# Performance work log

Measured on AMD Instinct MI355X. Metric: run time of the kernel, lower is better.

## Reference

```python
import jax, jax.numpy as jnp
import numpy as np


def _pairwise_l2(set1, set2):
    # set1: [B, N, C], set2: [B, M, C] -> [B, N, M] Euclidean distances.
    # Equivalent to ||a - b||_2 computed via the expanded quadratic form,
    # avoiding the O(B*N*M*C) broadcasted-difference intermediate.
    sq1 = jnp.sum(set1 * set1, axis=-1)  # [B, N]
    sq2 = jnp.sum(set2 * set2, axis=-1)  # [B, M]
    inner = jnp.einsum('bnc,bmc->bnm', set1, set2)  # [B, N, M]
    d2 = sq1[:, :, None] + sq2[:, None, :] - 2.0 * inner
    return jnp.sqrt(jnp.maximum(d2, 0.0))


def reference(set1, set2):
    # mode == Hausdorff.average
    if set1.ndim == 2:
        set1 = set1[None]
    if set2.ndim == 2:
        set2 = set2[None]
    distances = _pairwise_l2(set1, set2)  # [B, N, M]
    term_1 = jnp.mean(jnp.min(distances, axis=2), axis=1)  # [B]
    term_2 = jnp.mean(jnp.min(distances, axis=1), axis=1)  # [B]
    res = term_1 + term_2
    if res.shape[0] == 1:
        res = jnp.squeeze(res, axis=0)
    return res


def setup_inputs() -> dict:
    key = jax.random.key(0)
    k1, k2 = jax.random.split(key)
    B, N, M, C = 8, 4096, 4096, 128
    set1 = jax.random.normal(k1, (B, N, C), dtype=jnp.float32)
    set2 = jax.random.normal(k2, (B, M, C), dtype=jnp.float32)
    return {"set1": set1, "set2": set2}
```

## Files before the change

### kernel.cpp

```cpp
#include <hip/hip_runtime.h>

#define B_ 8
#define N_ 4096
#define M_ 4096
#define C_ 128
#define BN_ (B_ * N_)
#define BM_ (B_ * M_)

typedef __attribute__((ext_vector_type(8))) short bf16x8;
typedef __attribute__((ext_vector_type(4))) float floatx4;
typedef __attribute__((ext_vector_type(8))) unsigned short ushort8;

__device__ __forceinline__ unsigned short f2bf(float x) {
    unsigned int u = __float_as_uint(x);
    u += 0x7FFFu + ((u >> 16) & 1u);
    return (unsigned short)(u >> 16);
}

__device__ __forceinline__ void gl2lds16(const void* g, void* l) {
    __builtin_amdgcn_global_load_lds(
        (const __attribute__((address_space(1))) void*)g,
        (__attribute__((address_space(3))) void*)l, 16, 0, 0);
}

__global__ __launch_bounds__(256) void prep_kernel(
    const float* __restrict__ S1, const float* __restrict__ S2,
    unsigned int* __restrict__ minbuf, float* __restrict__ norms,
    unsigned short* __restrict__ bfA, unsigned short* __restrict__ bfB,
    float* __restrict__ out) {
    const int lane = threadIdx.x & 63;
    const int w    = threadIdx.x >> 6;
    const int gw   = blockIdx.x * 4 + w;
    const int r4   = lane >> 4;
    const int g4   = lane & 15;
    const int row  = gw * 4 + r4;

    const float* src = (row < BN_) ? S1 + (size_t)row * C_
                                   : S2 + (size_t)(row - BN_) * C_;
    float4 v0 = ((const float4*)src)[g4 * 2];
    float4 v1 = ((const float4*)src)[g4 * 2 + 1];

    float s = v0.x*v0.x + v0.y*v0.y + v0.z*v0.z + v0.w*v0.w
            + v1.x*v1.x + v1.y*v1.y + v1.z*v1.z + v1.w*v1.w;
    s += __shfl_xor(s, 1, 64);
    s += __shfl_xor(s, 2, 64);
    s += __shfl_xor(s, 4, 64);
    s += __shfl_xor(s, 8, 64);

    ushort8 o;
    o[0] = f2bf(v0.x); o[1] = f2bf(v0.y); o[2] = f2bf(v0.z); o[3] = f2bf(v0.w);
    o[4] = f2bf(v1.x); o[5] = f2bf(v1.y); o[6] = f2bf(v1.z); o[7] = f2bf(v1.w);

    unsigned short* dst = (row < BN_) ? bfA + (size_t)row * C_
                                      : bfB + (size_t)(row - BN_) * C_;
    *(ushort8*)&dst[(g4 ^ (row & 15)) * 8] = o;

    if (g4 == 0) { norms[row] = s; minbuf[row] = 0x7F800000u; }
    if (blockIdx.x == 0 && threadIdx.x < B_) out[threadIdx.x] = 0.f;
}

__global__ __launch_bounds__(256, 2) void hausdorff_mfma(
    const unsigned short* __restrict__ Abf, const unsigned short* __restrict__ Bbf,
    const float* __restrict__ asq_g, const float* __restrict__ bsq_g,
    unsigned int* __restrict__ rowmin, unsigned int* __restrict__ colmin) {

    __shared__ unsigned short B_lds[2][64 * 128];

    const int b     = blockIdx.z;
    const int row0  = blockIdx.x * 128;
    const int panel = blockIdx.y;
    const int tid   = threadIdx.x;
    const int lane  = tid & 63;
    const int w     = tid >> 6;
    const int lm    = lane & 15;
    const int quad  = lane >> 4;
    const int wrow  = (w >> 1) * 64;
    const int qc    = (w & 1) * 32;

    const unsigned short* Aws = Abf + ((size_t)b * N_ + row0) * C_;
    const unsigned short* Bws = Bbf + ((size_t)b * M_ + panel * 1024) * C_;

    #pragma unroll
    for (int k = 0; k < 4; ++k) {
        const int off = w * 2048 + k * 512;
        gl2lds16(Aws + off + lane * 8,        &B_lds[0][off]);
        gl2lds16(Aws + 8192 + off + lane * 8, &B_lds[1][off]);
    }

    float sa[16];
    #pragma unroll
    for (int i = 0; i < 4; ++i) {
        float4 t = *(const float4*)&asq_g[(size_t)b * N_ + row0 + wrow + 16 * i + 4 * quad];
        sa[4*i+0] = t.x; sa[4*i+1] = t.y; sa[4*i+2] = t.z; sa[4*i+3] = t.w;
    }

    float rv[16];
    #pragma unroll
    for (int v = 0; v < 16; ++v) rv[v] = 1e30f;

    __syncthreads();

    bf16x8 af[4][4];
    {
        const unsigned short* Abuf = &B_lds[w >> 1][0];
        #pragma unroll
        for (int i = 0; i < 4; ++i)
            #pragma unroll
            for (int c = 0; c < 4; ++c)
                af[i][c] = *(const bf16x8*)
                    &Abuf[(16 * i + lm) * 128 + (((c * 4 + quad) ^ lm) * 8)];
    }

    __syncthreads();

    #pragma unroll
    for (int k = 0; k < 4; ++k) {
        const int off = w * 2048 + k * 512;
        gl2lds16(Bws + off + lane * 8, &B_lds[0][off]);
    }
    __syncthreads();

    for (int it = 0; it < 16; ++it) {
        const int cur = it & 1;
        if (it < 15) {
            const unsigned short* Bt = Bws + (size_t)(it + 1) * 64 * C_;
            #pragma unroll
            for (int k = 0; k < 4; ++k) {
                const int off = w * 2048 + k * 512;
                gl2lds16(Bt + off + lane * 8, &B_lds[cur ^ 1][off]);
            }
        }
        const int colbase = panel * 1024 + it * 64;
        const float sb0 = bsq_g[(size_t)b * M_ + colbase + qc + lm];
        const float sb1 = bsq_g[(size_t)b * M_ + colbase + qc + 16 + lm];

        bf16x8 bf[2][4];
        #pragma unroll
        for (int j = 0; j < 2; ++j)
            #pragma unroll
            for (int c = 0; c < 4; ++c)
                bf[j][c] = *(const bf16x8*)
                    &B_lds[cur][(qc + 16 * j + lm) * 128 + (((c * 4 + quad) ^ lm) * 8)];

        floatx4 acc[4][2] = {};
        #pragma unroll
        for (int c = 0; c < 4; ++c)
            #pragma unroll
            for (int i = 0; i < 4; ++i)
                #pragma unroll
                for (int j = 0; j < 2; ++j)
                    acc[i][j] = __builtin_amdgcn_mfma_f32_16x16x32_bf16(
                        af[i][c], bf[j][c], acc[i][j], 0, 0, 0);

        float cv0 = 1e30f, cv1 = 1e30f;
        #pragma unroll
        for (int i = 0; i < 4; ++i)
            #pragma unroll
            for (int reg = 0; reg < 4; ++reg) {
                const int v = 4 * i + reg;
                float d0 = fmaf(-2.0f, acc[i][0][reg], sa[v] + sb0);
                float d1 = fmaf(-2.0f, acc[i][1][reg], sa[v] + sb1);
                rv[v] = fminf(rv[v], fminf(d0, d1));
                cv0 = fminf(cv0, d0);
                cv1 = fminf(cv1, d1);
            }
        cv0 = fminf(cv0, __shfl_xor(cv0, 16, 64));
        cv0 = fminf(cv0, __shfl_xor(cv0, 32, 64));
        cv1 = fminf(cv1, __shfl_xor(cv1, 16, 64));
        cv1 = fminf(cv1, __shfl_xor(cv1, 32, 64));
        if (quad == 0) {
            atomicMin(&colmin[(size_t)b * M_ + colbase + qc + lm],
                      __float_as_uint(fmaxf(cv0, 0.f)));
            atomicMin(&colmin[(size_t)b * M_ + colbase + qc + 16 + lm],
                      __float_as_uint(fmaxf(cv1, 0.f)));
        }
        __syncthreads();
    }

    #pragma unroll
    for (int s = 1; s < 16; s <<= 1)
        #pragma unroll
        for (int v = 0; v < 16; ++v)
            rv[v] = fminf(rv[v], __shfl_xor(rv[v], s, 64));
    if (lm == 0) {
        #pragma unroll
        for (int v = 0; v < 16; ++v)
            atomicMin(&rowmin[(size_t)b * N_ + row0 + wrow + 16 * (v >> 2) +
                              4 * quad + (v & 3)],
                      __float_as_uint(fmaxf(rv[v], 0.f)));
    }
}

__global__ __launch_bounds__(256) void hausdorff_reduce(
    const unsigned int* __restrict__ rowmin,
    const unsigned int* __restrict__ colmin, float* __restrict__ out) {
    __shared__ float ws4[4];
    const int b    = blockIdx.x >> 3;
    const int part = blockIdx.x & 7;
    const int base = part * 512;
    float s = 0.f;
    for (int i = base + threadIdx.x; i < base + 512; i += 256)
        s += sqrtf(fmaxf(__uint_as_float(rowmin[(size_t)b * N_ + i]), 0.f)) * (1.f / N_)
           + sqrtf(fmaxf(__uint_as_float(colmin[(size_t)b * M_ + i]), 0.f)) * (1.f / M_);
    #pragma unroll
    for (int off = 32; off > 0; off >>= 1) s += __shfl_down(s, off, 64);
    if ((threadIdx.x & 63) == 0) ws4[threadIdx.x >> 6] = s;
    __syncthreads();
    if (threadIdx.x == 0)
        atomicAdd(&out[b], ws4[0] + ws4[1] + ws4[2] + ws4[3]);
}

extern "C" void kernel_launch(void* const* d_in, const int* in_sizes, int n_in,
                              void* d_out, int out_size, void* d_ws, size_t ws_size,
                              hipStream_t stream) {
    const float* s1 = (const float*)d_in[0];
    const float* s2 = (const float*)d_in[1];
    float* out = (float*)d_out;

    unsigned int* rowmin = (unsigned int*)d_ws;
    unsigned int* colmin = rowmin + BN_;
    float* norms         = (float*)(colmin + BM_);
    unsigned short* bfA  = (unsigned short*)(norms + BN_ + BM_);
    unsigned short* bfB  = bfA + (size_t)BN_ * C_;

    prep_kernel<<<(BN_ + BM_) / 16, 256, 0, stream>>>(
        s1, s2, rowmin, norms, bfA, bfB, out);

    dim3 grid(N_ / 128, M_ / 1024, B_);
    hausdorff_mfma<<<grid, 256, 0, stream>>>(
        bfA, bfB, norms, norms + BN_, rowmin, colmin);

    hausdorff_reduce<<<B_ * 8, 256, 0, stream>>>(rowmin, colmin, out);
}
```

Measured before the change: 123.0 us.

## Fold norms into MFMA accumulator init, buffer column mins in LDS, fuse final reduce

The accumulators now start at -0.5*(|a|^2+|b|^2), so the MFMA directly produces a scaled negative squared distance. The epilogue becomes plain max operations instead of fma plus min. Per-tile column-min atomics go to an LDS buffer, which is flushed to global memory once per block, cutting global atomic traffic by 16x. A last-block-done counter per batch performs the final sqrt-mean reduction inside the main kernel, removing the third launch. The cost is a serialized tail reduction in one block per batch, plus the extra fence and counter logic.

```diff
diff --git a/kernel.cpp b/kernel.cpp
--- a/kernel.cpp
+++ b/kernel.cpp
@@ -27,7 +27,7 @@
     const float* __restrict__ S1, const float* __restrict__ S2,
     unsigned int* __restrict__ minbuf, float* __restrict__ norms,
     unsigned short* __restrict__ bfA, unsigned short* __restrict__ bfB,
-    float* __restrict__ out) {
+    float* __restrict__ out, unsigned int* __restrict__ done) {
     const int lane = threadIdx.x & 63;
     const int w    = threadIdx.x >> 6;
     const int gw   = blockIdx.x * 4 + w;
@@ -56,15 +56,22 @@
     *(ushort8*)&dst[(g4 ^ (row & 15)) * 8] = o;
 
     if (g4 == 0) { norms[row] = s; minbuf[row] = 0x7F800000u; }
-    if (blockIdx.x == 0 && threadIdx.x < B_) out[threadIdx.x] = 0.f;
+    if (blockIdx.x == 0 && threadIdx.x < B_) {
+        out[threadIdx.x] = 0.f;
+        done[threadIdx.x] = 0u;
+    }
 }
 
 __global__ __launch_bounds__(256, 2) void hausdorff_mfma(
     const unsigned short* __restrict__ Abf, const unsigned short* __restrict__ Bbf,
     const float* __restrict__ asq_g, const float* __restrict__ bsq_g,
-    unsigned int* __restrict__ rowmin, unsigned int* __restrict__ colmin) {
+    unsigned int* __restrict__ rowmin, unsigned int* __restrict__ colmin,
+    float* __restrict__ out, unsigned int* __restrict__ done_ctr) {
 
     __shared__ unsigned short B_lds[2][64 * 128];
+    __shared__ unsigned int colbuf[16 * 64];
+    __shared__ unsigned int s_last;
+    __shared__ float ws4[4];
 
     const int b     = blockIdx.z;
     const int row0  = blockIdx.x * 128;
@@ -87,16 +94,20 @@
         gl2lds16(Aws + 8192 + off + lane * 8, &B_lds[1][off]);
     }
 
-    float sa[16];
+    #pragma unroll
+    for (int e = 0; e < 4; ++e) colbuf[tid * 4 + e] = 0x7F800000u;
+
+    float sah[16];
     #pragma unroll
     for (int i = 0; i < 4; ++i) {
         float4 t = *(const float4*)&asq_g[(size_t)b * N_ + row0 + wrow + 16 * i + 4 * quad];
-        sa[4*i+0] = t.x; sa[4*i+1] = t.y; sa[4*i+2] = t.z; sa[4*i+3] = t.w;
+        sah[4*i+0] = -0.5f * t.x; sah[4*i+1] = -0.5f * t.y;
+        sah[4*i+2] = -0.5f * t.z; sah[4*i+3] = -0.5f * t.w;
     }
 
     float rv[16];
     #pragma unroll
-    for (int v = 0; v < 16; ++v) rv[v] = 1e30f;
+    for (int v = 0; v < 16; ++v) rv[v] = -1e30f;
 
     __syncthreads();
 
@@ -131,8 +142,8 @@
             }
         }
         const int colbase = panel * 1024 + it * 64;
-        const float sb0 = bsq_g[(size_t)b * M_ + colbase + qc + lm];
-        const float sb1 = bsq_g[(size_t)b * M_ + colbase + qc + 16 + lm];
+        const float nb0 = -0.5f * bsq_g[(size_t)b * M_ + colbase + qc + lm];
+        const float nb1 = -0.5f * bsq_g[(size_t)b * M_ + colbase + qc + 16 + lm];
 
         bf16x8 bf[2][4];
         #pragma unroll
@@ -142,7 +153,15 @@
                 bf[j][c] = *(const bf16x8*)
                     &B_lds[cur][(qc + 16 * j + lm) * 128 + (((c * 4 + quad) ^ lm) * 8)];
 
-        floatx4 acc[4][2] = {};
+        floatx4 acc[4][2];
+        #pragma unroll
+        for (int i = 0; i < 4; ++i)
+            #pragma unroll
+            for (int reg = 0; reg < 4; ++reg) {
+                acc[i][0][reg] = sah[4*i+reg] + nb0;
+                acc[i][1][reg] = sah[4*i+reg] + nb1;
+            }
+
         #pragma unroll
         for (int c = 0; c < 4; ++c)
             #pragma unroll
@@ -152,62 +171,75 @@
                     acc[i][j] = __builtin_amdgcn_mfma_f32_16x16x32_bf16(
                         af[i][c], bf[j][c], acc[i][j], 0, 0, 0);
 
-        float cv0 = 1e30f, cv1 = 1e30f;
-        #pragma unroll
-        for (int i = 0; i < 4; ++i)
-            #pragma unroll
-            for (int reg = 0; reg < 4; ++reg) {
-                const int v = 4 * i + reg;
-                float d0 = fmaf(-2.0f, acc[i][0][reg], sa[v] + sb0);
-                float d1 = fmaf(-2.0f, acc[i][1][reg], sa[v] + sb1);
-                rv[v] = fminf(rv[v], fminf(d0, d1));
-                cv0 = fminf(cv0, d0);
-                cv1 = fminf(cv1, d1);
-            }
-        cv0 = fminf(cv0, __shfl_xor(cv0, 16, 64));
-        cv0 = fminf(cv0, __shfl_xor(cv0, 32, 64));
-        cv1 = fminf(cv1, __shfl_xor(cv1, 16, 64));
-        cv1 = fminf(cv1, __shfl_xor(cv1, 32, 64));
+        float cv0 = -1e30f, cv1 = -1e30f;
+        #pragma unroll
+        for (int i = 0; i < 4; ++i) {
+            #pragma unroll
+            for (int reg = 0; reg < 4; ++reg)
+                rv[4*i+reg] = fmaxf(rv[4*i+reg],
+                                    fmaxf(acc[i][0][reg], acc[i][1][reg]));
+            cv0 = fmaxf(cv0, fmaxf(fmaxf(acc[i][0][0], acc[i][0][1]),
+                                   fmaxf(acc[i][0][2], acc[i][0][3])));
+            cv1 = fmaxf(cv1, fmaxf(fmaxf(acc[i][1][0], acc[i][1][1]),
+                                   fmaxf(acc[i][1][2], acc[i][1][3])));
+        }
+        cv0 = fmaxf(cv0, __shfl_xor(cv0, 16, 64));
+        cv0 = fmaxf(cv0, __shfl_xor(cv0, 32, 64));
+        cv1 = fmaxf(cv1, __shfl_xor(cv1, 16, 64));
+        cv1 = fmaxf(cv1, __shfl_xor(cv1, 32, 64));
         if (quad == 0) {
-            atomicMin(&colmin[(size_t)b * M_ + colbase + qc + lm],
-                      __float_as_uint(fmaxf(cv0, 0.f)));
-            atomicMin(&colmin[(size_t)b * M_ + colbase + qc + 16 + lm],
-                      __float_as_uint(fmaxf(cv1, 0.f)));
+            atomicMin(&colbuf[it * 64 + qc + lm],
+                      __float_as_uint(fmaxf(-2.0f * cv0, 0.f)));
+            atomicMin(&colbuf[it * 64 + qc + 16 + lm],
+                      __float_as_uint(fmaxf(-2.0f * cv1, 0.f)));
         }
         __syncthreads();
     }
 
     #pragma unroll
+    for (int e = 0; e < 4; ++e) {
+        const int idx = tid * 4 + e;
+        atomicMin(&colmin[(size_t)b * M_ + panel * 1024 + idx], colbuf[idx]);
+    }
+
+    #pragma unroll
     for (int s = 1; s < 16; s <<= 1)
         #pragma unroll
         for (int v = 0; v < 16; ++v)
-            rv[v] = fminf(rv[v], __shfl_xor(rv[v], s, 64));
+            rv[v] = fmaxf(rv[v], __shfl_xor(rv[v], s, 64));
     if (lm == 0) {
         #pragma unroll
         for (int v = 0; v < 16; ++v)
             atomicMin(&rowmin[(size_t)b * N_ + row0 + wrow + 16 * (v >> 2) +
                               4 * quad + (v & 3)],
-                      __float_as_uint(fmaxf(rv[v], 0.f)));
-    }
-}
-
-__global__ __launch_bounds__(256) void hausdorff_reduce(
-    const unsigned int* __restrict__ rowmin,
-    const unsigned int* __restrict__ colmin, float* __restrict__ out) {
-    __shared__ float ws4[4];
-    const int b    = blockIdx.x >> 3;
-    const int part = blockIdx.x & 7;
-    const int base = part * 512;
-    float s = 0.f;
-    for (int i = base + threadIdx.x; i < base + 512; i += 256)
-        s += sqrtf(fmaxf(__uint_as_float(rowmin[(size_t)b * N_ + i]), 0.f)) * (1.f / N_)
-           + sqrtf(fmaxf(__uint_as_float(colmin[(size_t)b * M_ + i]), 0.f)) * (1.f / M_);
-    #pragma unroll
-    for (int off = 32; off > 0; off >>= 1) s += __shfl_down(s, off, 64);
-    if ((threadIdx.x & 63) == 0) ws4[threadIdx.x >> 6] = s;
-    __syncthreads();
-    if (threadIdx.x == 0)
-        atomicAdd(&out[b], ws4[0] + ws4[1] + ws4[2] + ws4[3]);
+                      __float_as_uint(fmaxf(-2.0f * rv[v], 0.f)));
+    }
+
+    __syncthreads();
+    if (tid == 0) {
+        __threadfence();
+        s_last = (atomicAdd(&done_ctr[b], 1u) == 127u) ? 1u : 0u;
+    }
+    __syncthreads();
+    if (s_last) {
+        __threadfence();
+        float s = 0.f;
+        for (int i = tid; i < N_; i += 256) {
+            unsigned int ur = __hip_atomic_load(&rowmin[(size_t)b * N_ + i],
+                                                __ATOMIC_RELAXED,
+                                                __HIP_MEMORY_SCOPE_AGENT);
+            unsigned int uc = __hip_atomic_load(&colmin[(size_t)b * M_ + i],
+                                                __ATOMIC_RELAXED,
+                                                __HIP_MEMORY_SCOPE_AGENT);
+            s += sqrtf(fmaxf(__uint_as_float(ur), 0.f)) * (1.f / N_)
+               + sqrtf(fmaxf(__uint_as_float(uc), 0.f)) * (1.f / M_);
+        }
+        #pragma unroll
+        for (int off = 32; off > 0; off >>= 1) s += __shfl_down(s, off, 64);
+        if ((tid & 63) == 0) ws4[tid >> 6] = s;
+        __syncthreads();
+        if (tid == 0) out[b] = ws4[0] + ws4[1] + ws4[2] + ws4[3];
+    }
 }
 
 extern "C" void kernel_launch(void* const* d_in, const int* in_sizes, int n_in,
@@ -222,13 +254,12 @@
     float* norms         = (float*)(colmin + BM_);
     unsigned short* bfA  = (unsigned short*)(norms + BN_ + BM_);
     unsigned short* bfB  = bfA + (size_t)BN_ * C_;
+    unsigned int* done   = (unsigned int*)(bfB + (size_t)BM_ * C_);
 
     prep_kernel<<<(BN_ + BM_) / 16, 256, 0, stream>>>(
-        s1, s2, rowmin, norms, bfA, bfB, out);
+        s1, s2, rowmin, norms, bfA, bfB, out, done);
 
     dim3 grid(N_ / 128, M_ / 1024, B_);
     hausdorff_mfma<<<grid, 256, 0, stream>>>(
-        bfA, bfB, norms, norms + BN_, rowmin, colmin);
-
-    hausdorff_reduce<<<B_ * 8, 256, 0, stream>>>(rowmin, colmin, out);
-}
+        bfA, bfB, norms, norms + BN_, rowmin, colmin, out, done);
+}
```

Result: slower. 151.3 us (+23.0%).

## Buffer column minima in LDS and fuse final reduction via last-block counter

Applied to the files above, without the earlier changes.

Column minima from each tile are now stored in shared memory across all 16 iterations and merged once per block, so each block issues one atomicMin per column instead of two per 64-column tile per wave pair. The separate reduce kernel is removed: a per-batch completion counter lets the last finishing block compute the sqrt-mean sum and write the output. This removes a kernel launch and cuts global atomic traffic, in exchange for 8 KB more LDS per block (which may affect occupancy) and a serialized tail reduction done by one block per batch.

```diff
diff --git a/kernel.cpp b/kernel.cpp
--- a/kernel.cpp
+++ b/kernel.cpp
@@ -27,7 +27,7 @@
     const float* __restrict__ S1, const float* __restrict__ S2,
     unsigned int* __restrict__ minbuf, float* __restrict__ norms,
     unsigned short* __restrict__ bfA, unsigned short* __restrict__ bfB,
-    float* __restrict__ out) {
+    float* __restrict__ out, unsigned int* __restrict__ done) {
     const int lane = threadIdx.x & 63;
     const int w    = threadIdx.x >> 6;
     const int gw   = blockIdx.x * 4 + w;
@@ -56,15 +56,22 @@
     *(ushort8*)&dst[(g4 ^ (row & 15)) * 8] = o;
 
     if (g4 == 0) { norms[row] = s; minbuf[row] = 0x7F800000u; }
-    if (blockIdx.x == 0 && threadIdx.x < B_) out[threadIdx.x] = 0.f;
+    if (blockIdx.x == 0 && threadIdx.x < B_) {
+        out[threadIdx.x] = 0.f;
+        done[threadIdx.x] = 0u;
+    }
 }
 
 __global__ __launch_bounds__(256, 2) void hausdorff_mfma(
     const unsigned short* __restrict__ Abf, const unsigned short* __restrict__ Bbf,
     const float* __restrict__ asq_g, const float* __restrict__ bsq_g,
-    unsigned int* __restrict__ rowmin, unsigned int* __restrict__ colmin) {
+    unsigned int* __restrict__ rowmin, unsigned int* __restrict__ colmin,
+    float* __restrict__ out, unsigned int* __restrict__ done_ctr) {
 
     __shared__ unsigned short B_lds[2][64 * 128];
+    __shared__ unsigned int colbuf2[2][16 * 64];
+    unsigned int* s_last = &colbuf2[1][0];
+    float* ws4 = (float*)&colbuf2[0][0];
 
     const int b     = blockIdx.z;
     const int row0  = blockIdx.x * 128;
@@ -169,12 +176,17 @@
         cv1 = fminf(cv1, __shfl_xor(cv1, 16, 64));
         cv1 = fminf(cv1, __shfl_xor(cv1, 32, 64));
         if (quad == 0) {
-            atomicMin(&colmin[(size_t)b * M_ + colbase + qc + lm],
-                      __float_as_uint(fmaxf(cv0, 0.f)));
-            atomicMin(&colmin[(size_t)b * M_ + colbase + qc + 16 + lm],
-                      __float_as_uint(fmaxf(cv1, 0.f)));
+            colbuf2[w >> 1][it * 64 + qc + lm]      = __float_as_uint(fmaxf(cv0, 0.f));
+            colbuf2[w >> 1][it * 64 + qc + 16 + lm] = __float_as_uint(fmaxf(cv1, 0.f));
         }
         __syncthreads();
+    }
+
+    #pragma unroll
+    for (int e = 0; e < 4; ++e) {
+        const int idx = tid * 4 + e;
+        const unsigned int m = min(colbuf2[0][idx], colbuf2[1][idx]);
+        atomicMin(&colmin[(size_t)b * M_ + panel * 1024 + idx], m);
     }
 
     #pragma unroll
@@ -189,25 +201,33 @@
                               4 * quad + (v & 3)],
                       __float_as_uint(fmaxf(rv[v], 0.f)));
     }
-}
-
-__global__ __launch_bounds__(256) void hausdorff_reduce(
-    const unsigned int* __restrict__ rowmin,
-    const unsigned int* __restrict__ colmin, float* __restrict__ out) {
-    __shared__ float ws4[4];
-    const int b    = blockIdx.x >> 3;
-    const int part = blockIdx.x & 7;
-    const int base = part * 512;
-    float s = 0.f;
-    for (int i = base + threadIdx.x; i < base + 512; i += 256)
-        s += sqrtf(fmaxf(__uint_as_float(rowmin[(size_t)b * N_ + i]), 0.f)) * (1.f / N_)
-           + sqrtf(fmaxf(__uint_as_float(colmin[(size_t)b * M_ + i]), 0.f)) * (1.f / M_);
-    #pragma unroll
-    for (int off = 32; off > 0; off >>= 1) s += __shfl_down(s, off, 64);
-    if ((threadIdx.x & 63) == 0) ws4[threadIdx.x >> 6] = s;
-    __syncthreads();
-    if (threadIdx.x == 0)
-        atomicAdd(&out[b], ws4[0] + ws4[1] + ws4[2] + ws4[3]);
+
+    __syncthreads();
+    if (tid == 0) {
+        __threadfence();
+        *s_last = (atomicAdd(&done_ctr[b], 1u) == 127u) ? 1u : 0u;
+    }
+    __syncthreads();
+    if (*s_last) {
+        __threadfence();
+        float s = 0.f;
+        for (int i = tid; i < N_; i += 256) {
+            unsigned int ur = __hip_atomic_load(&rowmin[(size_t)b * N_ + i],
+                                                __ATOMIC_RELAXED,
+                                                __HIP_MEMORY_SCOPE_AGENT);
+            unsigned int uc = __hip_atomic_load(&colmin[(size_t)b * M_ + i],
+                                                __ATOMIC_RELAXED,
+                                                __HIP_MEMORY_SCOPE_AGENT);
+            s += sqrtf(fmaxf(__uint_as_float(ur), 0.f)) * (1.f / N_)
+               + sqrtf(fmaxf(__uint_as_float(uc), 0.f)) * (1.f / M_);
+        }
+        #pragma unroll
+        for (int off = 32; off > 0; off >>= 1) s += __shfl_down(s, off, 64);
+        __syncthreads();
+        if ((tid & 63) == 0) ws4[tid >> 6] = s;
+        __syncthreads();
+        if (tid == 0) out[b] = ws4[0] + ws4[1] + ws4[2] + ws4[3];
+    }
 }
 
 extern "C" void kernel_launch(void* const* d_in, const int* in_sizes, int n_in,
@@ -222,13 +242,12 @@
     float* norms         = (float*)(colmin + BM_);
     unsigned short* bfA  = (unsigned short*)(norms + BN_ + BM_);
     unsigned short* bfB  = bfA + (size_t)BN_ * C_;
+    unsigned int* done   = (unsigned int*)(bfB + (size_t)BM_ * C_);
 
     prep_kernel<<<(BN_ + BM_) / 16, 256, 0, stream>>>(
-        s1, s2, rowmin, norms, bfA, bfB, out);
+        s1, s2, rowmin, norms, bfA, bfB, out, done);
 
     dim3 grid(N_ / 128, M_ / 1024, B_);
     hausdorff_mfma<<<grid, 256, 0, stream>>>(
-        bfA, bfB, norms, norms + BN_, rowmin, colmin);
-
-    hausdorff_reduce<<<B_ * 8, 256, 0, stream>>>(rowmin, colmin, out);
-}
+        bfA, bfB, norms, norms + BN_, rowmin, colmin, out, done);
+}
```

After: 157.8 us. 28.3% more time.
